# Optimization experiments

Measured on AMD Instinct MI355X. Metric: run time of the kernel, lower is better.

Reference implementation:

```python
import jax, jax.numpy as jnp
import numpy as np

# Dimensions (production-scale molecular density evaluation)
S = 5        # n_species (element types)
NR = 3       # n_radial functions per element (max_funs)
NA = 3       # max_angular_moment -> l in {1,2,3}
F = NR * NA  # total terms (k=1)
B, M, N = 8, 4096, 64  # batch molecules, grid points, atoms
EPS = 1e-12


def setup_inputs() -> dict:
    key = jax.random.key(0)
    k1, k2, k3, k4, k5, k6 = jax.random.split(key, 6)
    dv = jax.random.normal(k1, (B, M, N, 3), jnp.float32)           # displacement grid_point - atom
    coefficients = jax.random.normal(k2, (B, N, F, 3), jnp.float32)  # per-atom anisotropic coeff vectors
    labels = jax.random.randint(k3, (B, N), 0, S)                    # species index per atom
    a = jax.random.uniform(k4, (S, NR), jnp.float32, 0.5, 2.0)       # amplitudes
    b = jax.random.uniform(k5, (S, NR), jnp.float32, 0.5, 3.0)       # exponents
    p = jax.random.uniform(k6, (S, NR), jnp.float32, 0.0, 2.0)       # radial powers
    return {"dv": dv, "coefficients": coefficients, "labels": labels, "a": a, "b": b, "p": p}


def _legendre(x, l):
    # Legendre polynomial P_l(x) for l in {1,2,3}; l broadcasts over the term dim
    p1 = x
    p2 = 0.5 * (3.0 * x * x - 1.0)
    p3 = 0.5 * (5.0 * x * x * x - 3.0 * x)
    return jnp.where(l == 1, p1, jnp.where(l == 2, p2, p3))


def reference(dv, coefficients, labels, a, b, p):
    # expand radial params across the angular terms (repeat_interleave along dim 1): [S, F]
    a_e = jnp.repeat(a, NA, axis=1)
    b_e = jnp.repeat(b, NA, axis=1)
    p_e = jnp.repeat(p, NA, axis=1)
    # per-atom label gather (expand_parameter): [B, N, F]
    a_g = a_e[labels]
    b_g = b_e[labels]
    p_g = p_e[labels]
    # distances: [B, M, N]
    r = jnp.linalg.norm(dv, axis=-1)
    r4 = r[..., None]                                   # [B, M, N, 1]
    # generalized exponential kernel a * r^p * exp(-b r): [B, M, N, F]
    kern = a_g[:, None] * r4 ** p_g[:, None] * jnp.exp(-b_g[:, None] * r4)
    # anisotropic angular part: |c| * P_l(cos angle(dv, c))
    cnorm = jnp.linalg.norm(coefficients, axis=-1)      # [B, N, F]
    cunit = coefficients / jnp.maximum(cnorm[..., None], EPS)
    cos = jnp.einsum('bmnd,bnfd->bmnf', dv, cunit) / jnp.maximum(r4, EPS)
    l_arr = (jnp.arange(F) % NA) + 1                    # 1,2,3 cycling (qi pattern)
    q = _legendre(cos, l_arr)                           # [B, M, N, F]
    dens = kern * cnorm[:, None] * q                    # [B, M, N, F]
    # accumulate over terms, then over atoms (density += k; density.sum(2))
    return dens.sum(axis=(2, 3))                        # [B, M]
```

## Files before the change

kernel.cpp:

```cpp
#include <hip/hip_runtime.h>

#define Bb  8
#define Mm  4096
#define Nn  64
#define Ff  9
#define Ss  5
#define NRr 3

constexpr int MT     = 32;
constexpr int NCHUNK = 8;
constexpr int APC    = 8;
constexpr int DV_PAD = 193;

__global__ __launch_bounds__(256, 4)
void HarmonicGenAMD_25786983645325_kernel(
    const float* __restrict__ dv,
    const float* __restrict__ coef,
    const int*   __restrict__ labels,
    const float* __restrict__ pa,
    const float* __restrict__ pb,
    const float* __restrict__ pp,
    float*       __restrict__ out)
{
    __shared__ __align__(16) float dvs[MT * DV_PAD];
    __shared__ __align__(16) float atomA[Nn * Ff * 4];
    __shared__ __align__(16) float atomR[Nn * NRr * 2];
    __shared__ float red[256];

    const int tid = threadIdx.x;
    const int blk = blockIdx.x;
    const int b   = blk >> 7;
    const int mt  = blk & 127;
    const int m0  = mt * MT;

    for (int i = tid; i < Nn * Ff; i += 256) {
        const int n  = i / Ff;
        const int f  = i - n * Ff;
        const int j  = f / 3;
        const int s  = labels[b * Nn + n];
        const float av = pa[s * NRr + j];
        const float bv = pb[s * NRr + j];
        const float pv = pp[s * NRr + j];
        const float* c = coef + ((size_t)(b * Nn + n) * Ff + f) * 3;
        const float cx = c[0], cy = c[1], cz = c[2];
        const float cn  = __builtin_amdgcn_sqrtf(cx * cx + cy * cy + cz * cz);
        const float inv = 1.0f / fmaxf(cn, 1e-12f);
        float* d = &atomA[i * 4];
        d[0] = av * cn;
        d[1] = cx * inv;
        d[2] = cy * inv;
        d[3] = cz * inv;
        if ((f - j * 3) == 0) {
            atomR[(n * NRr + j) * 2 + 0] = bv * 1.44269504088896340736f;
            atomR[(n * NRr + j) * 2 + 1] = pv;
        }
    }

    const float* g = dv + ((size_t)b * Mm + m0) * (Nn * 3);
    for (int i = tid * 4; i < MT * Nn * 3; i += 256 * 4) {
        const int row = i / 192;
        const int col = i - row * 192;
        const float4 v = *(const float4*)(g + (size_t)row * 192 + col);
        float* d = &dvs[row * DV_PAD + col];
        d[0] = v.x; d[1] = v.y; d[2] = v.z; d[3] = v.w;
    }
    __syncthreads();

    const int m_local = tid & 31;
    const int chunk   = tid >> 5;
    const float* drow = &dvs[m_local * DV_PAD + chunk * (APC * 3)];

    float acc = 0.0f;
#pragma unroll
    for (int n = 0; n < APC; ++n) {
        const float x = drow[n * 3 + 0];
        const float y = drow[n * 3 + 1];
        const float z = drow[n * 3 + 2];
        const float r2   = x * x + y * y + z * z;
        const float r    = __builtin_amdgcn_sqrtf(r2);
        const float rinv = __builtin_amdgcn_rcpf(fmaxf(r, 1e-12f));
        const float l2r  = 0.5f * __builtin_amdgcn_logf(r2);

        const int an = chunk * APC + n;
        const float* adA = &atomA[an * Ff * 4];
        const float* adR = &atomR[an * NRr * 2];
#pragma unroll
        for (int j = 0; j < 3; ++j) {
            const float Bc = adR[j * 2 + 0];
            const float P  = adR[j * 2 + 1];
            const float ek = __builtin_amdgcn_exp2f(__fmaf_rn(P, l2r, -Bc * r));
#pragma unroll
            for (int lm = 0; lm < 3; ++lm) {
                const float4 e4 = *(const float4*)&adA[(j * 3 + lm) * 4];
                const float kern = e4.x * ek;
                const float cosv = (x * e4.y + y * e4.z + z * e4.w) * rinv;
                float q;
                if (lm == 0)      q = cosv;
                else if (lm == 1) q = __fmaf_rn(1.5f * cosv, cosv, -0.5f);
                else              q = cosv * __fmaf_rn(2.5f * cosv, cosv, -1.5f);
                acc = __fmaf_rn(kern, q, acc);
            }
        }
    }

    red[tid] = acc;
    __syncthreads();
    if (tid < MT) {
        float s = 0.0f;
#pragma unroll
        for (int c = 0; c < NCHUNK; ++c) s += red[c * MT + tid];
        out[(size_t)b * Mm + m0 + tid] = s;
    }
}

extern "C" void kernel_launch(void* const* d_in, const int* in_sizes, int n_in,
                              void* d_out, int out_size, void* d_ws, size_t ws_size,
                              hipStream_t stream) {
    const float* dv   = (const float*)d_in[0];
    const float* coef = (const float*)d_in[1];
    const int*   lab  = (const int*)d_in[2];
    const float* pa   = (const float*)d_in[3];
    const float* pb   = (const float*)d_in[4];
    const float* pp   = (const float*)d_in[5];
    float* out = (float*)d_out;

    dim3 grid(Bb * (Mm / MT));
    HarmonicGenAMD_25786983645325_kernel<<<grid, 256, 0, stream>>>(
        dv, coef, lab, pa, pb, pp, out);
}
```

Before: 86.39 us.

## Precompute per-atom parameter table in separate kernel, read wave-uniform from global

Moves the per-atom coefficient normalisation and label gather out of every block into a small precompute kernel that writes 16-float records to workspace. The main kernel now uses 64 grid points per block, with each wave handling 16 atoms, so the table reads are wave-uniform and can become scalar loads. This removes redundant per-block setup and shared-memory staging, at the cost of a second launch, larger shared memory per block and lower occupancy (launch bounds 256,2).

```diff
diff --git a/kernel.cpp b/kernel.cpp
--- a/kernel.cpp
+++ b/kernel.cpp
@@ -7,72 +7,78 @@
 #define Ss  5
 #define NRr 3
 
-constexpr int MT     = 32;
-constexpr int NCHUNK = 8;
-constexpr int APC    = 8;
-constexpr int DV_PAD = 193;
+constexpr int REC = 16;
 
-__global__ __launch_bounds__(256, 4)
-void HarmonicGenAMD_25786983645325_kernel(
-    const float* __restrict__ dv,
+__global__ void HarmonicGen_precompute(
     const float* __restrict__ coef,
     const int*   __restrict__ labels,
     const float* __restrict__ pa,
     const float* __restrict__ pb,
     const float* __restrict__ pp,
+    float*       __restrict__ table)
+{
+    const int i = blockIdx.x * 256 + threadIdx.x;
+    if (i >= Bb * Nn * NRr) return;
+    const int j  = i % NRr;
+    const int bn = i / NRr;
+    const int s  = labels[bn];
+    const float av = pa[s * NRr + j];
+    const float bv = pb[s * NRr + j];
+    const float pv = pp[s * NRr + j];
+    float* rec = table + (size_t)i * REC;
+    rec[0] = bv * 1.44269504088896340736f;
+    rec[1] = pv;
+    rec[2] = 0.0f; rec[3] = 0.0f;
+#pragma unroll
+    for (int lm = 0; lm < 3; ++lm) {
+        const int f = j * 3 + lm;
+        const float* c = coef + ((size_t)bn * Ff + f) * 3;
+        const float cx = c[0], cy = c[1], cz = c[2];
+        const float cn  = sqrtf(cx * cx + cy * cy + cz * cz);
+        const float inv = 1.0f / fmaxf(cn, 1e-12f);
+        rec[4 + lm * 4 + 0] = av * cn;
+        rec[4 + lm * 4 + 1] = cx * inv;
+        rec[4 + lm * 4 + 2] = cy * inv;
+        rec[4 + lm * 4 + 3] = cz * inv;
+    }
+}
+
+constexpr int MT  = 64;
+constexpr int PAD = 193;
+
+__global__ __launch_bounds__(256, 2)
+void HarmonicGenAMD_25786983645325_kernel(
+    const float* __restrict__ dv,
+    const float* __restrict__ table,
     float*       __restrict__ out)
 {
-    __shared__ __align__(16) float dvs[MT * DV_PAD];
-    __shared__ __align__(16) float atomA[Nn * Ff * 4];
-    __shared__ __align__(16) float atomR[Nn * NRr * 2];
-    __shared__ float red[256];
+    __shared__ __align__(16) float dvs[MT * PAD];
+    __shared__ float red[4 * MT];
 
     const int tid = threadIdx.x;
     const int blk = blockIdx.x;
-    const int b   = blk >> 7;
-    const int mt  = blk & 127;
-    const int m0  = mt * MT;
-
-    for (int i = tid; i < Nn * Ff; i += 256) {
-        const int n  = i / Ff;
-        const int f  = i - n * Ff;
-        const int j  = f / 3;
-        const int s  = labels[b * Nn + n];
-        const float av = pa[s * NRr + j];
-        const float bv = pb[s * NRr + j];
-        const float pv = pp[s * NRr + j];
-        const float* c = coef + ((size_t)(b * Nn + n) * Ff + f) * 3;
-        const float cx = c[0], cy = c[1], cz = c[2];
-        const float cn  = __builtin_amdgcn_sqrtf(cx * cx + cy * cy + cz * cz);
-        const float inv = 1.0f / fmaxf(cn, 1e-12f);
-        float* d = &atomA[i * 4];
-        d[0] = av * cn;
-        d[1] = cx * inv;
-        d[2] = cy * inv;
-        d[3] = cz * inv;
-        if ((f - j * 3) == 0) {
-            atomR[(n * NRr + j) * 2 + 0] = bv * 1.44269504088896340736f;
-            atomR[(n * NRr + j) * 2 + 1] = pv;
-        }
-    }
+    const int b   = blk >> 6;
+    const int m0  = (blk & 63) * MT;
 
     const float* g = dv + ((size_t)b * Mm + m0) * (Nn * 3);
     for (int i = tid * 4; i < MT * Nn * 3; i += 256 * 4) {
         const int row = i / 192;
         const int col = i - row * 192;
         const float4 v = *(const float4*)(g + (size_t)row * 192 + col);
-        float* d = &dvs[row * DV_PAD + col];
+        float* d = &dvs[row * PAD + col];
         d[0] = v.x; d[1] = v.y; d[2] = v.z; d[3] = v.w;
     }
     __syncthreads();
 
-    const int m_local = tid & 31;
-    const int chunk   = tid >> 5;
-    const float* drow = &dvs[m_local * DV_PAD + chunk * (APC * 3)];
+    const int lane = tid & 63;
+    const int wid  = tid >> 6;
+    const float* drow = &dvs[lane * PAD];
+    const float4* tb = (const float4*)(table + (size_t)b * Nn * NRr * REC);
 
     float acc = 0.0f;
-#pragma unroll
-    for (int n = 0; n < APC; ++n) {
+#pragma unroll 4
+    for (int t = 0; t < 16; ++t) {
+        const int n = wid * 16 + t;
         const float x = drow[n * 3 + 0];
         const float y = drow[n * 3 + 1];
         const float z = drow[n * 3 + 2];
@@ -81,19 +87,16 @@
         const float rinv = __builtin_amdgcn_rcpf(fmaxf(r, 1e-12f));
         const float l2r  = 0.5f * __builtin_amdgcn_logf(r2);
 
-        const int an = chunk * APC + n;
-        const float* adA = &atomA[an * Ff * 4];
-        const float* adR = &atomR[an * NRr * 2];
+        const float4* rec = tb + (size_t)n * (NRr * 4);
 #pragma unroll
-        for (int j = 0; j < 3; ++j) {
-            const float Bc = adR[j * 2 + 0];
-            const float P  = adR[j * 2 + 1];
-            const float ek = __builtin_amdgcn_exp2f(__fmaf_rn(P, l2r, -Bc * r));
+        for (int j = 0; j < NRr; ++j) {
+            const float4 h = rec[j * 4 + 0];
+            const float ek = __builtin_amdgcn_exp2f(__fmaf_rn(h.y, l2r, -h.x * r));
 #pragma unroll
             for (int lm = 0; lm < 3; ++lm) {
-                const float4 e4 = *(const float4*)&adA[(j * 3 + lm) * 4];
-                const float kern = e4.x * ek;
-                const float cosv = (x * e4.y + y * e4.z + z * e4.w) * rinv;
+                const float4 e = rec[j * 4 + 1 + lm];
+                const float kern = e.x * ek;
+                const float cosv = (x * e.y + y * e.z + z * e.w) * rinv;
                 float q;
                 if (lm == 0)      q = cosv;
                 else if (lm == 1) q = __fmaf_rn(1.5f * cosv, cosv, -0.5f);
@@ -103,12 +106,10 @@
         }
     }
 
-    red[tid] = acc;
+    red[wid * MT + lane] = acc;
     __syncthreads();
     if (tid < MT) {
-        float s = 0.0f;
-#pragma unroll
-        for (int c = 0; c < NCHUNK; ++c) s += red[c * MT + tid];
+        const float s = red[tid] + red[MT + tid] + red[2 * MT + tid] + red[3 * MT + tid];
         out[(size_t)b * Mm + m0 + tid] = s;
     }
 }
@@ -122,9 +123,12 @@
     const float* pa   = (const float*)d_in[3];
     const float* pb   = (const float*)d_in[4];
     const float* pp   = (const float*)d_in[5];
-    float* out = (float*)d_out;
+    float* out   = (float*)d_out;
+    float* table = (float*)d_ws;
+
+    HarmonicGen_precompute<<<(Bb * Nn * NRr + 255) / 256, 256, 0, stream>>>(
+        coef, lab, pa, pb, pp, table);
 
     dim3 grid(Bb * (Mm / MT));
-    HarmonicGenAMD_25786983645325_kernel<<<grid, 256, 0, stream>>>(
-        dv, coef, lab, pa, pb, pp, out);
+    HarmonicGenAMD_25786983645325_kernel<<<grid, 256, 0, stream>>>(dv, table, out);
 }
```

Measured after the change: 95.67 us. 1.11x slower.
